# Kernel tuning notes

Hardware: AMD Instinct MI355X
Metric: run time of the kernel (lower is better)

The kernel has to match this reference:

```python
import jax, jax.numpy as jnp
import numpy as np

D_MODEL = 2048
NUM_HEADS = 16
D_K = D_MODEL // NUM_HEADS
ROPE_THETA = 10000.0
B, S = 2, 2048


def setup_inputs() -> dict:
    key = jax.random.key(0)
    ks = jax.random.split(key, 5)
    std = 1.0 / np.sqrt(D_MODEL)
    return {
        "x": jax.random.normal(ks[0], (B, S, D_MODEL), jnp.float32),
        "wq": jax.random.normal(ks[1], (D_MODEL, D_MODEL), jnp.float32) * std,
        "wk": jax.random.normal(ks[2], (D_MODEL, D_MODEL), jnp.float32) * std,
        "wv": jax.random.normal(ks[3], (D_MODEL, D_MODEL), jnp.float32) * std,
        "wo": jax.random.normal(ks[4], (D_MODEL, D_MODEL), jnp.float32) * std,
        "token_positions": jnp.arange(S, dtype=jnp.int32),
    }


def _rope(x, positions):
    # x: [b, h, s, d_k]; positions: [s]
    inv_freq = 1.0 / (ROPE_THETA ** (jnp.arange(0, D_K, 2, dtype=jnp.float32) / D_K))
    freqs = positions.astype(jnp.float32)[:, None] * inv_freq[None, :]  # [s, d_k/2]
    cos, sin = jnp.cos(freqs), jnp.sin(freqs)
    x_even, x_odd = x[..., ::2], x[..., 1::2]
    out_even = x_even * cos - x_odd * sin
    out_odd = x_even * sin + x_odd * cos
    # re-interleave even/odd lanes
    return jnp.stack([out_even, out_odd], axis=-1).reshape(x.shape)


def reference(x, wq, wk, wv, wo, token_positions):
    b, s, _ = x.shape
    # projections: weight is [out, in] as in torch Linear-style einsum
    q = jnp.einsum("bsd,ed->bse", x, wq)
    k = jnp.einsum("bsd,ed->bse", x, wk)
    v = jnp.einsum("bsd,ed->bse", x, wv)
    # split heads: b s (h d) -> b h s d
    def split(t):
        return t.reshape(b, s, NUM_HEADS, D_K).transpose(0, 2, 1, 3)
    q, k, v = split(q), split(k), split(v)
    q = _rope(q, token_positions)
    k = _rope(k, token_positions)
    scores = jnp.einsum("bhmd,bhnd->bhmn", q, k) / jnp.sqrt(jnp.float32(D_K))
    causal = jnp.tril(jnp.ones((s, s), dtype=bool))
    scores = jnp.where(causal[None, None], scores, -jnp.inf)
    attn = jax.nn.softmax(scores, axis=-1)
    out = jnp.einsum("bhmn,bhnd->bhmd", attn, v)
    out = out.transpose(0, 2, 1, 3).reshape(b, s, D_MODEL)
    return jnp.einsum("em,bsm->bse", wo, out)
```

## Files before the change

### kernel.cpp

```cpp
#include <hip/hip_runtime.h>

#define S_LEN 2048
#define DM 2048
#define NH 16
#define DK 128
#define BB 2
#define BH (BB*NH)
#define GK 2048

typedef float f32x4 __attribute__((ext_vector_type(4)));
typedef __bf16 bf16x8 __attribute__((ext_vector_type(8)));
typedef __bf16 bf16x4 __attribute__((ext_vector_type(4)));
typedef unsigned int u32;

#define AS1 __attribute__((address_space(1)))
#define AS3 __attribute__((address_space(3)))

__device__ inline void gload16(const void* g, void* l){
  __builtin_amdgcn_global_load_lds((AS1 const u32*)g, (AS3 u32*)l, 16, 0, 0);
}

__device__ inline ushort f2bf(float f){
  __bf16 h = (__bf16)f;
  ushort u;
  __builtin_memcpy(&u, &h, 2);
  return u;
}

__global__ void k_f32_to_bf16(const float* __restrict__ in, ushort* __restrict__ out, int n4){
  int i = blockIdx.x * blockDim.x + threadIdx.x;
  if (i >= n4) return;
  float4 v = reinterpret_cast<const float4*>(in)[i];
  ushort4 o;
  o.x = f2bf(v.x); o.y = f2bf(v.y); o.z = f2bf(v.z); o.w = f2bf(v.w);
  reinterpret_cast<ushort4*>(out)[i] = o;
}

__global__ void k_w4(const float* __restrict__ wq, const float* __restrict__ wk,
                     const float* __restrict__ wv, const float* __restrict__ wo4,
                     ushort* __restrict__ dqkv, ushort* __restrict__ dwo){
  int i = blockIdx.x * 256 + threadIdx.x;
  int sel = i >> 20;
  int off = i & ((1 << 20) - 1);
  const float* s = (sel == 0) ? wq : (sel == 1) ? wk : (sel == 2) ? wv : wo4;
  ushort* d = (sel < 3) ? (dqkv + (size_t)sel * DM * DM) : dwo;
  float4 v = reinterpret_cast<const float4*>(s)[off];
  ushort4 o;
  o.x = f2bf(v.x); o.y = f2bf(v.y); o.z = f2bf(v.z); o.w = f2bf(v.w);
  reinterpret_cast<ushort4*>(d)[off] = o;
}

__global__ void k_rope_table(const int* __restrict__ pos, float2* __restrict__ cs){
  int idx = blockIdx.x * 256 + threadIdx.x;
  if (idx >= S_LEN * 64) return;
  int s = idx >> 6, i = idx & 63;
  float inv = expf(-0.14391156831212787f * (float)i);
  float f = (float)pos[s] * inv;
  cs[idx] = make_float2(cosf(f), sinf(f));
}

#define SBAR() do{ __builtin_amdgcn_s_barrier(); __builtin_amdgcn_sched_barrier(0); }while(0)
#define VMC(n) asm volatile("s_waitcnt vmcnt(" #n ")" ::: "memory")

#define STG(slot, srcp, tks, khh) do{ \
  const ushort* _s = (srcp) + (tks)*64 + (khh)*32; \
  gload16(_s,                    lds + (slot)*8192 + wid*512); \
  gload16(_s + (size_t)128*GK,   lds + (slot)*8192 + 4096 + wid*512); \
}while(0)

#define RD_A(slot, mh) do{ \
  af[0] = *reinterpret_cast<const bf16x8*>(ldsc + (slot)*16384 + wm*8192 + ((mh)*4+0)*1024 + frA); \
  af[1] = *reinterpret_cast<const bf16x8*>(ldsc + (slot)*16384 + wm*8192 + ((mh)*4+1)*1024 + frA); \
  af[2] = *reinterpret_cast<const bf16x8*>(ldsc + (slot)*16384 + wm*8192 + ((mh)*4+2)*1024 + frA); \
  af[3] = *reinterpret_cast<const bf16x8*>(ldsc + (slot)*16384 + wm*8192 + ((mh)*4+3)*1024 + frA); \
}while(0)

#define RD_B(slot) do{ \
  bfr[0] = *reinterpret_cast<const bf16x8*>(ldsc + (slot)*16384 + wn*4096 + 0*1024 + frA); \
  bfr[1] = *reinterpret_cast<const bf16x8*>(ldsc + (slot)*16384 + wn*4096 + 1*1024 + frA); \
  bfr[2] = *reinterpret_cast<const bf16x8*>(ldsc + (slot)*16384 + wn*4096 + 2*1024 + frA); \
  bfr[3] = *reinterpret_cast<const bf16x8*>(ldsc + (slot)*16384 + wn*4096 + 3*1024 + frA); \
}while(0)

#define MM(mh) do{ \
  __builtin_amdgcn_s_setprio(1); \
  _Pragma("unroll") \
  for (int mf2 = 0; mf2 < 4; mf2++) \
    _Pragma("unroll") \
    for (int nf = 0; nf < 4; nf++) \
      acc[(mh)*4+mf2][nf] = __builtin_amdgcn_mfma_f32_16x16x32_bf16(af[mf2], bfr[nf], acc[(mh)*4+mf2][nf], 0, 0, 0); \
  __builtin_amdgcn_s_setprio(0); \
}while(0)

__launch_bounds__(512, 2)
__global__ void k_gemm_qk(const ushort* __restrict__ A, const ushort* __restrict__ Bt,
                          const float2* __restrict__ cs,
                          ushort* __restrict__ Qh, ushort* __restrict__ Kh){
  __shared__ short lds[65536];
  const int tid = threadIdx.x, lane = tid & 63, wid = tid >> 6;
  const int wm = wid >> 2, wn = wid & 3;
  const int fr = lane & 15, fq = lane >> 4;

  const int bid = blockIdx.x;
  const int b2 = (bid & 7) * 32 + (bid >> 3);
  const int by = b2 >> 4, bx = b2 & 15;

  const int rbase = wid * 16 + (lane >> 2);
  const int kup = ((lane & 3) ^ ((lane >> 3) & 3)) * 8;
  const ushort* pa = A  + (size_t)(by * 256 + rbase) * GK + kup;
  const ushort* pb = Bt + (size_t)(bx * 256 + rbase) * GK + kup;

  const char* ldsc = (const char*)lds;
  const int frA = fr * 64 + ((fq * 16) ^ (((fr >> 1) & 3) << 4));

  f32x4 acc[8][4] = {};
  bf16x8 af[4], bfr[4];

  STG(0, pa, 0, 0); STG(1, pb, 0, 0); STG(2, pa, 0, 1); STG(3, pb, 0, 1);
  STG(4, pa, 1, 0); STG(5, pb, 1, 0);
  VMC(8);
  SBAR();

  #pragma unroll 1
  for (int it = 0; it < 16; ++it){
    const int tb  = 2 * it + 1;
    const int tn  = (2 * it + 2 < 32) ? 2 * it + 2 : 31;
    const int tn1 = (2 * it + 3 < 32) ? 2 * it + 3 : 31;
    RD_A(0, 0); RD_B(1); STG(6, pa, tb, 1);           SBAR(); MM(0); SBAR();
    RD_A(0, 1);          STG(7, pb, tb, 1);  VMC(6);  SBAR(); MM(1); SBAR();
    RD_A(2, 0); RD_B(3); STG(0, pa, tn, 0);           SBAR(); MM(0); SBAR();
    RD_A(2, 1);          STG(1, pb, tn, 0);  VMC(6);  SBAR(); MM(1); SBAR();
    RD_A(4, 0); RD_B(5); STG(2, pa, tn, 1);           SBAR(); MM(0); SBAR();
    RD_A(4, 1);          STG(3, pb, tn, 1);  VMC(6);  SBAR(); MM(1); SBAR();
    RD_A(6, 0); RD_B(7); STG(4, pa, tn1, 0);          SBAR(); MM(0); SBAR();
    RD_A(6, 1);          STG(5, pb, tn1, 0); VMC(6);  SBAR(); MM(1); SBAR();
  }

  const int rowb = by * 256 + wm * 128 + fq * 4;
  const bool isQ = (bx < 8);
  ushort* dst = isQ ? Qh : Kh;
  const float qscl = isQ ? 0.08838834764831845f : 1.0f;
  #pragma unroll
  for (int mf = 0; mf < 8; mf++)
    #pragma unroll
    for (int nf = 0; nf < 4; nf++){
      int col = bx * 256 + wn * 64 + nf * 16 + fr;
      int cg = col & 2047;
      int hh = cg >> 7, dd = cg & 127, jj = (cg >> 1) & 63;
      #pragma unroll
      for (int i = 0; i < 4; i++){
        int row = rowb + mf * 16 + i;
        int s = row & (S_LEN - 1), bb = row >> 11;
        float2 c2 = cs[s * 64 + jj];
        float v = acc[mf][nf][i];
        float p = __shfl_xor(v, 1);
        float o = (fr & 1) ? fmaf(p, c2.y, v * c2.x) : fmaf(v, c2.x, -p * c2.y);
        dst[((size_t)(bb * NH + hh) * S_LEN + s) * DK + dd] = f2bf(o * qscl);
      }
    }
}

#define WSTG_A(si, tks, khh) do{ \
  const ushort* _s = pa + (tks)*64 + (khh)*32; \
  gload16(_s,                  lds + (si)*8192 + wid*512); \
  gload16(_s + (size_t)128*GK, lds + (si)*8192 + 4096 + wid*512); \
}while(0)
#define WSTG_B(si, tks, khh) do{ \
  const ushort* _s = pb + (tks)*64 + (khh)*32; \
  gload16(_s, lds + 32768 + (si)*4096 + wid*512); \
}while(0)
#define WRD_A(si, mhf) do{ \
  af[0] = *reinterpret_cast<const bf16x8*>(ldsc + (si)*16384 + wm*4096 + ((mhf)*2+0)*1024 + frA); \
  af[1] = *reinterpret_cast<const bf16x8*>(ldsc + (si)*16384 + wm*4096 + ((mhf)*2+1)*1024 + frA); \
}while(0)
#define WRD_B(si) do{ \
  bfr[0] = *reinterpret_cast<const bf16x8*>(ldsc + 65536 + (si)*8192 + wn*4096 + 0*1024 + frA); \
  bfr[1] = *reinterpret_cast<const bf16x8*>(ldsc + 65536 + (si)*8192 + wn*4096 + 1*1024 + frA); \
  bfr[2] = *reinterpret_cast<const bf16x8*>(ldsc + 65536 + (si)*8192 + wn*4096 + 2*1024 + frA); \
  bfr[3] = *reinterpret_cast<const bf16x8*>(ldsc + 65536 + (si)*8192 + wn*4096 + 3*1024 + frA); \
}while(0)
#define WMM(mhf) do{ \
  __builtin_amdgcn_s_setprio(1); \
  _Pragma("unroll") \
  for (int k2 = 0; k2 < 2; k2++) \
    _Pragma("unroll") \
    for (int nf = 0; nf < 4; nf++) \
      acc[(mhf)*2+k2][nf] = __builtin_amdgcn_mfma_f32_16x16x32_bf16(af[k2], bfr[nf], acc[(mhf)*2+k2][nf], 0, 0, 0); \
  __builtin_amdgcn_s_setprio(0); \
}while(0)

#define WBODY() \
  WSTG_A(0, 0, 0); WSTG_B(0, 0, 0); WSTG_A(1, 0, 1); WSTG_B(1, 0, 1); \
  WSTG_A(2, 1, 0); WSTG_B(2, 1, 0); \
  VMC(6); \
  SBAR(); \
  _Pragma("unroll 1") \
  for (int it = 0; it < 16; ++it){ \
    const int tb  = 2 * it + 1; \
    const int tn  = (2 * it + 2 < 32) ? 2 * it + 2 : 31; \
    const int tn1 = (2 * it + 3 < 32) ? 2 * it + 3 : 31; \
    WRD_A(0, 0); WRD_B(0); WSTG_A(3, tb, 1);            SBAR(); WMM(0); SBAR(); \
    WRD_A(0, 1);           WSTG_B(3, tb, 1);  VMC(6);   SBAR(); WMM(1); SBAR(); \
    WRD_A(1, 0); WRD_B(1); WSTG_A(0, tn, 0);            SBAR(); WMM(0); SBAR(); \
    WRD_A(1, 1);           WSTG_B(0, tn, 0);  VMC(6);   SBAR(); WMM(1); SBAR(); \
    WRD_A(2, 0); WRD_B(2); WSTG_A(1, tn, 1);            SBAR(); WMM(0); SBAR(); \
    WRD_A(2, 1);           WSTG_B(1, tn, 1);  VMC(6);   SBAR(); WMM(1); SBAR(); \
    WRD_A(3, 0); WRD_B(3); WSTG_A(2, tn1, 0);           SBAR(); WMM(0); SBAR(); \
    WRD_A(3, 1);           WSTG_B(2, tn1, 0); VMC(6);   SBAR(); WMM(1); SBAR(); \
  }

__launch_bounds__(512, 2)
__global__ void k_gemm_v(const ushort* __restrict__ A, const ushort* __restrict__ Bt,
                         ushort* __restrict__ Vt){
  __shared__ short lds[49152];
  const int tid = threadIdx.x, lane = tid & 63, wid = tid >> 6;
  const int wm = wid >> 1, wn = wid & 1;
  const int fr = lane & 15, fq = lane >> 4;

  const int bid = blockIdx.x;
  const int b2 = (bid & 7) * 32 + (bid >> 3);
  const int by = b2 >> 4, bx = b2 & 15;

  const int rbase = wid * 16 + (lane >> 2);
  const int kup = ((lane & 3) ^ ((lane >> 3) & 3)) * 8;
  const ushort* pa = A  + (size_t)(by * 256 + rbase) * GK + kup;
  const ushort* pb = Bt + (size_t)(bx * 128 + rbase) * GK + kup;

  const char* ldsc = (const char*)lds;
  const int frA = fr * 64 + ((fq * 16) ^ (((fr >> 1) & 3) << 4));

  f32x4 acc[4][4] = {};
  bf16x8 af[2], bfr[4];

  WBODY();

  const int rowb = by * 256 + wm * 64 + fq * 4;
  #pragma unroll
  for (int mf = 0; mf < 4; mf++){
    int row0 = rowb + mf * 16;
    int s0 = row0 & (S_LEN - 1), bb = row0 >> 11;
    #pragma unroll
    for (int nf = 0; nf < 4; nf++){
      int col = bx * 128 + wn * 64 + nf * 16 + fr;
      int hh = col >> 7, dd = col & 127;
      ushort4 o;
      o.x = f2bf(acc[mf][nf][0]); o.y = f2bf(acc[mf][nf][1]);
      o.z = f2bf(acc[mf][nf][2]); o.w = f2bf(acc[mf][nf][3]);
      *reinterpret_cast<ushort4*>(&Vt[((size_t)(bb * NH + hh) * DK + dd) * S_LEN + s0]) = o;
    }
  }
}

__launch_bounds__(512, 2)
__global__ void k_gemm_wo(const ushort* __restrict__ A, const ushort* __restrict__ Bt,
                          float* __restrict__ C){
  __shared__ short lds[49152];
  const int tid = threadIdx.x, lane = tid & 63, wid = tid >> 6;
  const int wm = wid >> 1, wn = wid & 1;
  const int fr = lane & 15, fq = lane >> 4;

  const int bid = blockIdx.x;
  const int b2 = (bid & 7) * 32 + (bid >> 3);
  const int by = b2 >> 4, bx = b2 & 15;

  const int rbase = wid * 16 + (lane >> 2);
  const int kup = ((lane & 3) ^ ((lane >> 3) & 3)) * 8;
  const ushort* pa = A  + (size_t)(by * 256 + rbase) * GK + kup;
  const ushort* pb = Bt + (size_t)(bx * 128 + rbase) * GK + kup;

  const char* ldsc = (const char*)lds;
  const int frA = fr * 64 + ((fq * 16) ^ (((fr >> 1) & 3) << 4));

  f32x4 acc[4][4] = {};
  bf16x8 af[2], bfr[4];

  WBODY();

  const int orow = by * 256 + wm * 64 + fq * 4;
  const int ocol = bx * 128 + wn * 64 + fr;
  #pragma unroll
  for (int mf = 0; mf < 4; mf++)
    #pragma unroll
    for (int nf = 0; nf < 4; nf++)
      #pragma unroll
      for (int i = 0; i < 4; i++)
        C[(size_t)(orow + mf * 16 + i) * DM + ocol + nf * 16] = acc[mf][nf][i];
}

__launch_bounds__(512)
__global__ void k_attn(const ushort* __restrict__ Q, const ushort* __restrict__ K,
                       const ushort* __restrict__ Vt, ushort* __restrict__ O){
  __shared__ short Kt[2][64 * 128];
  __shared__ short Vl[2][128 * 64];
  __shared__ short Pl[8][16 * 80];
  const int tid = threadIdx.x, lane = tid & 63, wid = tid >> 6;
  const int bid = blockIdx.x;
  const int pid = bid >> 5;
  const int bh = bid & 31;
  const int b = bh >> 4, h = bh & 15;
  const int fr = lane & 15, fq = lane >> 4;
  const int swz = (fr & 7) << 4;

  const ushort* kb = K  + (size_t)bh * S_LEN * DK;
  const ushort* vb = Vt + (size_t)bh * DK * S_LEN;
  char* PlB = (char*)Pl + wid * 2560;
  ushort* ob = O + (size_t)b * S_LEN * DM;

  int kro[2], kco[2], vro[2], vco[2];
  #pragma unroll
  for (int jj = 0; jj < 2; jj++){
    int ins = wid * 2 + jj;
    kro[jj] = ins * 4 + (lane >> 4);
    kco[jj] = 8 * ((lane & 15) ^ (kro[jj] & 7));
    vro[jj] = ins * 8 + (lane >> 3);
    vco[jj] = 8 * ((lane & 7) ^ (vro[jj] & 7));
  }

  #pragma unroll 1
  for (int half = 0; half < 2; half++){
    const int j = half ? pid : 15 - pid;
    const int qr = j * 128 + wid * 16;
    const int nt = 2 * j + 2;

    bf16x8 qf[4];
    #pragma unroll
    for (int c = 0; c < 4; c++)
      qf[c] = *reinterpret_cast<const bf16x8*>(
          Q + ((size_t)bh * S_LEN + qr + fr) * DK + c * 32 + fq * 8);

    float mi = -1e30f, li = 0.f;
    f32x4 accO[8] = {};

    __syncthreads();
    #pragma unroll
    for (int jj = 0; jj < 2; jj++){
      int ins = wid * 2 + jj;
      gload16(kb + (size_t)kro[jj] * DK + kco[jj],      (char*)Kt + ins * 1024);
      gload16(vb + (size_t)vro[jj] * S_LEN + vco[jj],   (char*)Vl + ins * 1024);
    }
    __syncthreads();

    #pragma unroll 1
    for (int kt = 0; kt < nt; kt++){
      const int k0 = kt * 64;
      const int cur = kt & 1;
      if (kt + 1 < nt){
        const int k1 = k0 + 64;
        #pragma unroll
        for (int jj = 0; jj < 2; jj++){
          int ins = wid * 2 + jj;
          gload16(kb + (size_t)(k1 + kro[jj]) * DK + kco[jj],  (char*)Kt + (cur ^ 1) * 16384 + ins * 1024);
          gload16(vb + (size_t)vro[jj] * S_LEN + k1 + vco[jj], (char*)Vl + (cur ^ 1) * 16384 + ins * 1024);
        }
      }
      const char* KtB = (const char*)Kt + cur * 16384;
      const char* VlB = (const char*)Vl + cur * 16384;

      f32x4 sc[4] = {};
      #pragma unroll
      for (int c = 0; c < 4; c++){
        bf16x8 kf[4];
        #pragma unroll
        for (int ch = 0; ch < 4; ch++)
          kf[ch] = *reinterpret_cast<const bf16x8*>(
              KtB + (ch * 16 + fr) * 256 + ((c * 64 + fq * 16) ^ swz));
        #pragma unroll
        for (int ch = 0; ch < 4; ch++)
          sc[ch] = __builtin_amdgcn_mfma_f32_16x16x32_bf16(kf[ch], qf[c], sc[ch], 0, 0, 0);
      }

      const int qrow = qr + fr;
      if (k0 + 63 > qr){
        #pragma unroll
        for (int ch = 0; ch < 4; ch++)
          #pragma unroll
          for (int i = 0; i < 4; i++)
            if (k0 + ch * 16 + fq * 4 + i > qrow) sc[ch][i] = -1e30f;
      }

      float mx = sc[0][0];
      #pragma unroll
      for (int ch = 0; ch < 4; ch++)
        #pragma unroll
        for (int i = 0; i < 4; i++) mx = fmaxf(mx, sc[ch][i]);
      mx = fmaxf(mx, __shfl_xor(mx, 16));
      mx = fmaxf(mx, __shfl_xor(mx, 32));

      if (!__all(mx <= mi + 8.0f)){
        float mn = fmaxf(mi, mx);
        float scl = __expf(mi - mn);
        mi = mn;
        li *= scl;
        float sclq[4];
        #pragma unroll
        for (int i = 0; i < 4; i++) sclq[i] = __shfl(scl, fq * 4 + i);
        #pragma unroll
        for (int dt = 0; dt < 8; dt++)
          #pragma unroll
          for (int i = 0; i < 4; i++) accO[dt][i] *= sclq[i];
      }

      float rs = 0.f;
      #pragma unroll
      for (int ch = 0; ch < 4; ch++)
        #pragma unroll
        for (int i = 0; i < 4; i++){
          float e = __expf(sc[ch][i] - mi);
          sc[ch][i] = e;
          rs += e;
        }
      rs += __shfl_xor(rs, 16);
      rs += __shfl_xor(rs, 32);
      li += rs;

      #pragma unroll
      for (int ch = 0; ch < 4; ch++){
        bf16x4 pk;
        pk[0] = (__bf16)sc[ch][0]; pk[1] = (__bf16)sc[ch][1];
        pk[2] = (__bf16)sc[ch][2]; pk[3] = (__bf16)sc[ch][3];
        *reinterpret_cast<bf16x4*>(PlB + fr * 160 + ch * 32 + fq * 8) = pk;
      }
      bf16x8 pf[2];
      #pragma unroll
      for (int c2 = 0; c2 < 2; c2++)
        pf[c2] = *reinterpret_cast<const bf16x8*>(PlB + fr * 160 + c2 * 64 + fq * 16);

      #pragma unroll
      for (int dt = 0; dt < 8; dt++)
        #pragma unroll
        for (int c2 = 0; c2 < 2; c2++){
          bf16x8 vf = *reinterpret_cast<const bf16x8*>(
              VlB + (dt * 16 + fr) * 128 + ((c2 * 64 + fq * 16) ^ swz));
          accO[dt] = __builtin_amdgcn_mfma_f32_16x16x32_bf16(pf[c2], vf, accO[dt], 0, 0, 0);
        }
      __syncthreads();
    }

    float inv[4];
    #pragma unroll
    for (int i = 0; i < 4; i++) inv[i] = 1.f / __shfl(li, fq * 4 + i);
    #pragma unroll
    for (int dt = 0; dt < 8; dt++)
      #pragma unroll
      for (int i = 0; i < 4; i++){
        int row = qr + fq * 4 + i;
        ob[(size_t)row * DM + h * DK + dt * 16 + fr] = f2bf(accO[dt][i] * inv[i]);
      }
  }
}

extern "C" void kernel_launch(void* const* d_in, const int* in_sizes, int n_in,
                              void* d_out, int out_size, void* d_ws, size_t ws_size,
                              hipStream_t stream){
  const float* x  = (const float*)d_in[0];
  const float* wq = (const float*)d_in[1];
  const float* wk = (const float*)d_in[2];
  const float* wv = (const float*)d_in[3];
  const float* wo = (const float*)d_in[4];
  const int* pos  = (const int*)d_in[5];
  float* out = (float*)d_out;

  char* ws = (char*)d_ws;
  ushort* xb   = (ushort*)(ws);
  ushort* Ob   = xb;
  ushort* wqkv = (ushort*)(ws + 16777216);
  ushort* Qh   = (ushort*)(ws + 41943040);
  ushort* Kh   = (ushort*)(ws + 58720256);
  ushort* Vt   = (ushort*)(ws + 75497472);
  float2* cs   = (float2*)(ws + 92274688);
  ushort* wob  = (ushort*)(ws + 93323264);

  const int M = BB * S_LEN;

  k_rope_table<<<(S_LEN * 64) / 256, 256, 0, stream>>>(pos, cs);
  k_f32_to_bf16<<<(M * DM / 4) / 256, 256, 0, stream>>>(x, xb, M * DM / 4);
  k_w4<<<4 * (DM * DM / 4) / 256, 256, 0, stream>>>(wq, wk, wv, wo, wqkv, wob);

  k_gemm_qk<<<256, 512, 0, stream>>>(xb, wqkv, cs, Qh, Kh);
  k_gemm_v<<<256, 512, 0, stream>>>(xb, wqkv + (size_t)2 * DM * DM, Vt);

  k_attn<<<256, 512, 0, stream>>>(Qh, Kh, Vt, Ob);

  k_gemm_wo<<<256, 512, 0, stream>>>(Ob, wob, out);
}
```

Measured before the change: 246.6 us.

## Rewrite attention kernel with 32x32 MFMA and register-level P shuffle

Attention now uses 32x32x16 bf16 MFMA tiles, with each wave owning 32 query rows instead of 16. The P matrix is reshaped for the PV MFMA through cross-lane shuffles, removing the LDS round trip. The launch changes to 512 blocks of 256 threads, each handling a single 128-row query tile, instead of 256 blocks of 512 threads each handling a pair of causal-balanced tiles. This aims to cut LDS traffic and instruction count per FLOP. It raises register pressure and drops the explicit pairing of long and short causal tiles within a block.

```diff
diff --git a/kernel.cpp b/kernel.cpp
--- a/kernel.cpp
+++ b/kernel.cpp
@@ -9,8 +9,9 @@
 #define GK 2048
 
 typedef float f32x4 __attribute__((ext_vector_type(4)));
+typedef float f32x16 __attribute__((ext_vector_type(16)));
 typedef __bf16 bf16x8 __attribute__((ext_vector_type(8)));
-typedef __bf16 bf16x4 __attribute__((ext_vector_type(4)));
+typedef __bf16 bf16x2 __attribute__((ext_vector_type(2)));
 typedef unsigned int u32;
 
 #define AS1 __attribute__((address_space(1)))
@@ -25,6 +26,11 @@
   ushort u;
   __builtin_memcpy(&u, &h, 2);
   return u;
+}
+
+__device__ inline u32 cvtpk(float a, float b){
+  bf16x2 p; p[0] = (__bf16)a; p[1] = (__bf16)b;
+  u32 r; __builtin_memcpy(&r, &p, 4); return r;
 }
 
 __global__ void k_f32_to_bf16(const float* __restrict__ in, ushort* __restrict__ out, int n4){
@@ -287,166 +293,165 @@
         C[(size_t)(orow + mf * 16 + i) * DM + ocol + nf * 16] = acc[mf][nf][i];
 }
 
-__launch_bounds__(512)
+__launch_bounds__(256, 2)
 __global__ void k_attn(const ushort* __restrict__ Q, const ushort* __restrict__ K,
                        const ushort* __restrict__ Vt, ushort* __restrict__ O){
   __shared__ short Kt[2][64 * 128];
   __shared__ short Vl[2][128 * 64];
-  __shared__ short Pl[8][16 * 80];
   const int tid = threadIdx.x, lane = tid & 63, wid = tid >> 6;
   const int bid = blockIdx.x;
-  const int pid = bid >> 5;
-  const int bh = bid & 31;
-  const int b = bh >> 4, h = bh & 15;
-  const int fr = lane & 15, fq = lane >> 4;
-  const int swz = (fr & 7) << 4;
-
-  const ushort* kb = K  + (size_t)bh * S_LEN * DK;
-  const ushort* vb = Vt + (size_t)bh * DK * S_LEN;
-  char* PlB = (char*)Pl + wid * 2560;
+  const int bh = bid & 31, b = bh >> 4, hh = bh & 15;
+  const int t8 = (bid >> 5) & 7;
+  const int j = (bid < 256) ? (15 - t8) : t8;
+  const int nt = 2 * j + 2;
+  const int ql = lane & 31, h = lane >> 5;
+  const int qrb = j * 128 + wid * 32;
+  const int qrow = qrb + ql;
+  const int swz = (ql & 7) << 4;
+
+  const ushort* kbp = K  + (size_t)bh * S_LEN * DK;
+  const ushort* vbp = Vt + (size_t)bh * DK * S_LEN;
   ushort* ob = O + (size_t)b * S_LEN * DM;
 
-  int kro[2], kco[2], vro[2], vco[2];
-  #pragma unroll
-  for (int jj = 0; jj < 2; jj++){
-    int ins = wid * 2 + jj;
+  int kro[4], kco[4], vro[4], vco[4];
+  #pragma unroll
+  for (int jj = 0; jj < 4; jj++){
+    int ins = wid * 4 + jj;
     kro[jj] = ins * 4 + (lane >> 4);
     kco[jj] = 8 * ((lane & 15) ^ (kro[jj] & 7));
     vro[jj] = ins * 8 + (lane >> 3);
     vco[jj] = 8 * ((lane & 7) ^ (vro[jj] & 7));
   }
 
+  bf16x8 qf[8];
+  #pragma unroll
+  for (int s = 0; s < 8; s++)
+    qf[s] = *reinterpret_cast<const bf16x8*>(
+        Q + ((size_t)bh * S_LEN + qrow) * DK + s * 16 + h * 8);
+
+  float mi = -1e30f, li = 0.f;
+  f32x16 accO[4] = {};
+
+  #pragma unroll
+  for (int jj = 0; jj < 4; jj++){
+    int ins = wid * 4 + jj;
+    gload16(kbp + (size_t)kro[jj] * DK + kco[jj],      (char*)Kt + ins * 1024);
+    gload16(vbp + (size_t)vro[jj] * S_LEN + vco[jj],   (char*)Vl + ins * 1024);
+  }
+  __syncthreads();
+
   #pragma unroll 1
-  for (int half = 0; half < 2; half++){
-    const int j = half ? pid : 15 - pid;
-    const int qr = j * 128 + wid * 16;
-    const int nt = 2 * j + 2;
-
-    bf16x8 qf[4];
-    #pragma unroll
-    for (int c = 0; c < 4; c++)
-      qf[c] = *reinterpret_cast<const bf16x8*>(
-          Q + ((size_t)bh * S_LEN + qr + fr) * DK + c * 32 + fq * 8);
-
-    float mi = -1e30f, li = 0.f;
-    f32x4 accO[8] = {};
-
+  for (int kt = 0; kt < nt; kt++){
+    const int k0 = kt * 64;
+    const int cur = kt & 1;
+    if (kt + 1 < nt){
+      const int k1 = k0 + 64;
+      #pragma unroll
+      for (int jj = 0; jj < 4; jj++){
+        int ins = wid * 4 + jj;
+        gload16(kbp + (size_t)(k1 + kro[jj]) * DK + kco[jj],  (char*)Kt + (cur ^ 1) * 16384 + ins * 1024);
+        gload16(vbp + (size_t)vro[jj] * S_LEN + k1 + vco[jj], (char*)Vl + (cur ^ 1) * 16384 + ins * 1024);
+      }
+    }
+    const char* KtB = (const char*)Kt + cur * 16384;
+    const char* VlB = (const char*)Vl + cur * 16384;
+
+    f32x16 sc[2] = {};
+    #pragma unroll
+    for (int s = 0; s < 8; s++){
+      bf16x8 kf0 = *reinterpret_cast<const bf16x8*>(
+          KtB + (ql) * 256 + ((s * 32 + h * 16) ^ swz));
+      bf16x8 kf1 = *reinterpret_cast<const bf16x8*>(
+          KtB + (32 + ql) * 256 + ((s * 32 + h * 16) ^ swz));
+      sc[0] = __builtin_amdgcn_mfma_f32_32x32x16_bf16(kf0, qf[s], sc[0], 0, 0, 0);
+      sc[1] = __builtin_amdgcn_mfma_f32_32x32x16_bf16(kf1, qf[s], sc[1], 0, 0, 0);
+    }
+
+    if (k0 + 63 > qrb){
+      #pragma unroll
+      for (int kb = 0; kb < 2; kb++)
+        #pragma unroll
+        for (int r = 0; r < 16; r++)
+          if (k0 + kb * 32 + (r & 3) + 8 * (r >> 2) + 4 * h > qrow) sc[kb][r] = -1e30f;
+    }
+
+    float mx = sc[0][0];
+    #pragma unroll
+    for (int kb = 0; kb < 2; kb++)
+      #pragma unroll
+      for (int r = 0; r < 16; r++) mx = fmaxf(mx, sc[kb][r]);
+    mx = fmaxf(mx, __shfl_xor(mx, 32));
+
+    if (!__all(mx <= mi + 8.0f)){
+      float mn = fmaxf(mi, mx);
+      float scl = __expf(mi - mn);
+      mi = mn;
+      li *= scl;
+      float sclr[16];
+      #pragma unroll
+      for (int r = 0; r < 16; r++) sclr[r] = __shfl(scl, (r & 3) + 8 * (r >> 2) + 4 * h);
+      #pragma unroll
+      for (int dt = 0; dt < 4; dt++)
+        #pragma unroll
+        for (int r = 0; r < 16; r++) accO[dt][r] *= sclr[r];
+    }
+
+    float rs = 0.f;
+    #pragma unroll
+    for (int kb = 0; kb < 2; kb++)
+      #pragma unroll
+      for (int r = 0; r < 16; r++){
+        float e = __expf(sc[kb][r] - mi);
+        sc[kb][r] = e;
+        rs += e;
+      }
+    rs += __shfl_xor(rs, 32);
+    li += rs;
+
+    bf16x8 pf[4];
+    #pragma unroll
+    for (int t = 0; t < 4; t++){
+      const int kbb = t >> 1, rb = (t & 1) * 8;
+      u32 wA0 = cvtpk(sc[kbb][rb + 0], sc[kbb][rb + 1]);
+      u32 wA1 = cvtpk(sc[kbb][rb + 2], sc[kbb][rb + 3]);
+      u32 wB0 = cvtpk(sc[kbb][rb + 4], sc[kbb][rb + 5]);
+      u32 wB1 = cvtpk(sc[kbb][rb + 6], sc[kbb][rb + 7]);
+      u32 X = h ? wA0 : wB0;
+      u32 Y = h ? wA1 : wB1;
+      u32 x0 = (u32)__shfl_xor((int)X, 32);
+      u32 x1 = (u32)__shfl_xor((int)Y, 32);
+      u32 f[4];
+      f[0] = h ? x0 : wA0;
+      f[1] = h ? x1 : wA1;
+      f[2] = h ? wB0 : x0;
+      f[3] = h ? wB1 : x1;
+      __builtin_memcpy(&pf[t], f, 16);
+    }
+
+    #pragma unroll
+    for (int dt = 0; dt < 4; dt++){
+      const int vrow = dt * 32 + ql;
+      const int vswz = (vrow & 7) << 4;
+      #pragma unroll
+      for (int t = 0; t < 4; t++){
+        bf16x8 vf = *reinterpret_cast<const bf16x8*>(
+            VlB + vrow * 128 + ((t * 32 + h * 16) ^ vswz));
+        accO[dt] = __builtin_amdgcn_mfma_f32_32x32x16_bf16(pf[t], vf, accO[dt], 0, 0, 0);
+      }
+    }
     __syncthreads();
-    #pragma unroll
-    for (int jj = 0; jj < 2; jj++){
-      int ins = wid * 2 + jj;
-      gload16(kb + (size_t)kro[jj] * DK + kco[jj],      (char*)Kt + ins * 1024);
-      gload16(vb + (size_t)vro[jj] * S_LEN + vco[jj],   (char*)Vl + ins * 1024);
-    }
-    __syncthreads();
-
-    #pragma unroll 1
-    for (int kt = 0; kt < nt; kt++){
-      const int k0 = kt * 64;
-      const int cur = kt & 1;
-      if (kt + 1 < nt){
-        const int k1 = k0 + 64;
-        #pragma unroll
-        for (int jj = 0; jj < 2; jj++){
-          int ins = wid * 2 + jj;
-          gload16(kb + (size_t)(k1 + kro[jj]) * DK + kco[jj],  (char*)Kt + (cur ^ 1) * 16384 + ins * 1024);
-          gload16(vb + (size_t)vro[jj] * S_LEN + k1 + vco[jj], (char*)Vl + (cur ^ 1) * 16384 + ins * 1024);
-        }
-      }
-      const char* KtB = (const char*)Kt + cur * 16384;
-      const char* VlB = (const char*)Vl + cur * 16384;
-
-      f32x4 sc[4] = {};
-      #pragma unroll
-      for (int c = 0; c < 4; c++){
-        bf16x8 kf[4];
-        #pragma unroll
-        for (int ch = 0; ch < 4; ch++)
-          kf[ch] = *reinterpret_cast<const bf16x8*>(
-              KtB + (ch * 16 + fr) * 256 + ((c * 64 + fq * 16) ^ swz));
-        #pragma unroll
-        for (int ch = 0; ch < 4; ch++)
-          sc[ch] = __builtin_amdgcn_mfma_f32_16x16x32_bf16(kf[ch], qf[c], sc[ch], 0, 0, 0);
-      }
-
-      const int qrow = qr + fr;
-      if (k0 + 63 > qr){
-        #pragma unroll
-        for (int ch = 0; ch < 4; ch++)
-          #pragma unroll
-          for (int i = 0; i < 4; i++)
-            if (k0 + ch * 16 + fq * 4 + i > qrow) sc[ch][i] = -1e30f;
-      }
-
-      float mx = sc[0][0];
-      #pragma unroll
-      for (int ch = 0; ch < 4; ch++)
-        #pragma unroll
-        for (int i = 0; i < 4; i++) mx = fmaxf(mx, sc[ch][i]);
-      mx = fmaxf(mx, __shfl_xor(mx, 16));
-      mx = fmaxf(mx, __shfl_xor(mx, 32));
-
-      if (!__all(mx <= mi + 8.0f)){
-        float mn = fmaxf(mi, mx);
-        float scl = __expf(mi - mn);
-        mi = mn;
-        li *= scl;
-        float sclq[4];
-        #pragma unroll
-        for (int i = 0; i < 4; i++) sclq[i] = __shfl(scl, fq * 4 + i);
-        #pragma unroll
-        for (int dt = 0; dt < 8; dt++)
-          #pragma unroll
-          for (int i = 0; i < 4; i++) accO[dt][i] *= sclq[i];
-      }
-
-      float rs = 0.f;
-      #pragma unroll
-      for (int ch = 0; ch < 4; ch++)
-        #pragma unroll
-        for (int i = 0; i < 4; i++){
-          float e = __expf(sc[ch][i] - mi);
-          sc[ch][i] = e;
-          rs += e;
-        }
-      rs += __shfl_xor(rs, 16);
-      rs += __shfl_xor(rs, 32);
-      li += rs;
-
-      #pragma unroll
-      for (int ch = 0; ch < 4; ch++){
-        bf16x4 pk;
-        pk[0] = (__bf16)sc[ch][0]; pk[1] = (__bf16)sc[ch][1];
-        pk[2] = (__bf16)sc[ch][2]; pk[3] = (__bf16)sc[ch][3];
-        *reinterpret_cast<bf16x4*>(PlB + fr * 160 + ch * 32 + fq * 8) = pk;
-      }
-      bf16x8 pf[2];
-      #pragma unroll
-      for (int c2 = 0; c2 < 2; c2++)
-        pf[c2] = *reinterpret_cast<const bf16x8*>(PlB + fr * 160 + c2 * 64 + fq * 16);
-
-      #pragma unroll
-      for (int dt = 0; dt < 8; dt++)
-        #pragma unroll
-        for (int c2 = 0; c2 < 2; c2++){
-          bf16x8 vf = *reinterpret_cast<const bf16x8*>(
-              VlB + (dt * 16 + fr) * 128 + ((c2 * 64 + fq * 16) ^ swz));
-          accO[dt] = __builtin_amdgcn_mfma_f32_16x16x32_bf16(pf[c2], vf, accO[dt], 0, 0, 0);
-        }
-      __syncthreads();
-    }
-
-    float inv[4];
-    #pragma unroll
-    for (int i = 0; i < 4; i++) inv[i] = 1.f / __shfl(li, fq * 4 + i);
-    #pragma unroll
-    for (int dt = 0; dt < 8; dt++)
-      #pragma unroll
-      for (int i = 0; i < 4; i++){
-        int row = qr + fq * 4 + i;
-        ob[(size_t)row * DM + h * DK + dt * 16 + fr] = f2bf(accO[dt][i] * inv[i]);
-      }
-  }
+  }
+
+  float invr[16];
+  #pragma unroll
+  for (int r = 0; r < 16; r++) invr[r] = 1.f / __shfl(li, (r & 3) + 8 * (r >> 2) + 4 * h);
+  #pragma unroll
+  for (int dt = 0; dt < 4; dt++)
+    #pragma unroll
+    for (int r = 0; r < 16; r++){
+      int row = qrb + (r & 3) + 8 * (r >> 2) + 4 * h;
+      ob[(size_t)row * DM + hh * DK + dt * 32 + ql] = f2bf(accO[dt][r] * invr[r]);
+    }
 }
 
 extern "C" void kernel_launch(void* const* d_in, const int* in_sizes, int n_in,
@@ -479,7 +484,7 @@
   k_gemm_qk<<<256, 512, 0, stream>>>(xb, wqkv, cs, Qh, Kh);
   k_gemm_v<<<256, 512, 0, stream>>>(xb, wqkv + (size_t)2 * DM * DM, Vt);
 
-  k_attn<<<256, 512, 0, stream>>>(Qh, Kh, Vt, Ob);
+  k_attn<<<512, 256, 0, stream>>>(Qh, Kh, Vt, Ob);
 
   k_gemm_wo<<<256, 512, 0, stream>>>(Ob, wob, out);
 }
```

Measured after the change: 247.8 us. About the same (+0.5%).

## Split attention into 64-row query tiles with 256-thread blocks; merge conversion kernels

Applied to the files above, without the earlier changes.

The attention kernel now uses 4 waves per block covering 64 query rows instead of 8 waves covering 128. It launches 512 blocks paired for causal load balance, and each wave loads twice as many K/V chunks. Masking is applied only on the diagonal tile. The x and weight fp32-to-bf16 conversions are merged into one launch to save a kernel launch. Smaller blocks give finer work granularity and aim for two blocks per CU, at the cost of more K/V loads per query.

```diff
diff --git a/kernel.cpp b/kernel.cpp
--- a/kernel.cpp
+++ b/kernel.cpp
@@ -27,23 +27,20 @@
   return u;
 }
 
-__global__ void k_f32_to_bf16(const float* __restrict__ in, ushort* __restrict__ out, int n4){
-  int i = blockIdx.x * blockDim.x + threadIdx.x;
-  if (i >= n4) return;
-  float4 v = reinterpret_cast<const float4*>(in)[i];
-  ushort4 o;
-  o.x = f2bf(v.x); o.y = f2bf(v.y); o.z = f2bf(v.z); o.w = f2bf(v.w);
-  reinterpret_cast<ushort4*>(out)[i] = o;
-}
-
-__global__ void k_w4(const float* __restrict__ wq, const float* __restrict__ wk,
-                     const float* __restrict__ wv, const float* __restrict__ wo4,
-                     ushort* __restrict__ dqkv, ushort* __restrict__ dwo){
+__global__ void k_conv(const float* __restrict__ x, const float* __restrict__ wq,
+                       const float* __restrict__ wk, const float* __restrict__ wv,
+                       const float* __restrict__ wo4,
+                       ushort* __restrict__ xb, ushort* __restrict__ dqkv,
+                       ushort* __restrict__ dwo){
   int i = blockIdx.x * 256 + threadIdx.x;
   int sel = i >> 20;
   int off = i & ((1 << 20) - 1);
-  const float* s = (sel == 0) ? wq : (sel == 1) ? wk : (sel == 2) ? wv : wo4;
-  ushort* d = (sel < 3) ? (dqkv + (size_t)sel * DM * DM) : dwo;
+  const float* s; ushort* d;
+  if (sel < 2){ s = x + ((size_t)sel << 22); d = xb + ((size_t)sel << 22); }
+  else if (sel == 2){ s = wq; d = dqkv; }
+  else if (sel == 3){ s = wk; d = dqkv + (size_t)DM * DM; }
+  else if (sel == 4){ s = wv; d = dqkv + (size_t)2 * DM * DM; }
+  else { s = wo4; d = dwo; }
   float4 v = reinterpret_cast<const float4*>(s)[off];
   ushort4 o;
   o.x = f2bf(v.x); o.y = f2bf(v.y); o.z = f2bf(v.z); o.w = f2bf(v.w);
@@ -287,12 +284,12 @@
         C[(size_t)(orow + mf * 16 + i) * DM + ocol + nf * 16] = acc[mf][nf][i];
 }
 
-__launch_bounds__(512)
+__launch_bounds__(256, 2)
 __global__ void k_attn(const ushort* __restrict__ Q, const ushort* __restrict__ K,
                        const ushort* __restrict__ Vt, ushort* __restrict__ O){
   __shared__ short Kt[2][64 * 128];
   __shared__ short Vl[2][128 * 64];
-  __shared__ short Pl[8][16 * 80];
+  __shared__ short Pl[4][16 * 80];
   const int tid = threadIdx.x, lane = tid & 63, wid = tid >> 6;
   const int bid = blockIdx.x;
   const int pid = bid >> 5;
@@ -306,10 +303,10 @@
   char* PlB = (char*)Pl + wid * 2560;
   ushort* ob = O + (size_t)b * S_LEN * DM;
 
-  int kro[2], kco[2], vro[2], vco[2];
+  int kro[4], kco[4], vro[4], vco[4];
   #pragma unroll
-  for (int jj = 0; jj < 2; jj++){
-    int ins = wid * 2 + jj;
+  for (int jj = 0; jj < 4; jj++){
+    int ins = wid * 4 + jj;
     kro[jj] = ins * 4 + (lane >> 4);
     kco[jj] = 8 * ((lane & 15) ^ (kro[jj] & 7));
     vro[jj] = ins * 8 + (lane >> 3);
@@ -318,9 +315,9 @@
 
   #pragma unroll 1
   for (int half = 0; half < 2; half++){
-    const int j = half ? pid : 15 - pid;
-    const int qr = j * 128 + wid * 16;
-    const int nt = 2 * j + 2;
+    const int j = half ? pid : 31 - pid;
+    const int qr = j * 64 + wid * 16;
+    const int nt = j + 1;
 
     bf16x8 qf[4];
     #pragma unroll
@@ -332,11 +329,15 @@
     f32x4 accO[8] = {};
 
     __syncthreads();
-    #pragma unroll
-    for (int jj = 0; jj < 2; jj++){
-      int ins = wid * 2 + jj;
-      gload16(kb + (size_t)kro[jj] * DK + kco[jj],      (char*)Kt + ins * 1024);
-      gload16(vb + (size_t)vro[jj] * S_LEN + vco[jj],   (char*)Vl + ins * 1024);
+    {
+      char* kd = (char*)Kt;
+      char* vd = (char*)Vl;
+      #pragma unroll
+      for (int jj = 0; jj < 4; jj++){
+        int ins = wid * 4 + jj;
+        gload16(kb + (size_t)kro[jj] * DK + kco[jj],      kd + ins * 1024);
+        gload16(vb + (size_t)vro[jj] * S_LEN + vco[jj],   vd + ins * 1024);
+      }
     }
     __syncthreads();
 
@@ -346,11 +347,13 @@
       const int cur = kt & 1;
       if (kt + 1 < nt){
         const int k1 = k0 + 64;
-        #pragma unroll
-        for (int jj = 0; jj < 2; jj++){
-          int ins = wid * 2 + jj;
-          gload16(kb + (size_t)(k1 + kro[jj]) * DK + kco[jj],  (char*)Kt + (cur ^ 1) * 16384 + ins * 1024);
-          gload16(vb + (size_t)vro[jj] * S_LEN + k1 + vco[jj], (char*)Vl + (cur ^ 1) * 16384 + ins * 1024);
+        char* kd = (char*)Kt + (cur ^ 1) * 16384;
+        char* vd = (char*)Vl + (cur ^ 1) * 16384;
+        #pragma unroll
+        for (int jj = 0; jj < 4; jj++){
+          int ins = wid * 4 + jj;
+          gload16(kb + (size_t)(k1 + kro[jj]) * DK + kco[jj],  kd + ins * 1024);
+          gload16(vb + (size_t)vro[jj] * S_LEN + k1 + vco[jj], vd + ins * 1024);
         }
       }
       const char* KtB = (const char*)Kt + cur * 16384;
@@ -370,7 +373,7 @@
       }
 
       const int qrow = qr + fr;
-      if (k0 + 63 > qr){
+      if (kt == nt - 1){
         #pragma unroll
         for (int ch = 0; ch < 4; ch++)
           #pragma unroll
@@ -470,16 +473,13 @@
   float2* cs   = (float2*)(ws + 92274688);
   ushort* wob  = (ushort*)(ws + 93323264);
 
-  const int M = BB * S_LEN;
-
   k_rope_table<<<(S_LEN * 64) / 256, 256, 0, stream>>>(pos, cs);
-  k_f32_to_bf16<<<(M * DM / 4) / 256, 256, 0, stream>>>(x, xb, M * DM / 4);
-  k_w4<<<4 * (DM * DM / 4) / 256, 256, 0, stream>>>(wq, wk, wv, wo, wqkv, wob);
+  k_conv<<<24576, 256, 0, stream>>>(x, wq, wk, wv, wo, xb, wqkv, wob);
 
   k_gemm_qk<<<256, 512, 0, stream>>>(xb, wqkv, cs, Qh, Kh);
   k_gemm_v<<<256, 512, 0, stream>>>(xb, wqkv + (size_t)2 * DM * DM, Vt);
 
-  k_attn<<<256, 512, 0, stream>>>(Qh, Kh, Vt, Ob);
+  k_attn<<<512, 256, 0, stream>>>(Qh, Kh, Vt, Ob);
 
   k_gemm_wo<<<256, 512, 0, stream>>>(Ob, wob, out);
 }
```

After: 243.4 us. Within noise of the previous version (-1.3%).
